# Performance work log

Hardware: AMD Instinct MI355X
Metric: run time of the kernel (lower is better)

The kernel has to match this reference:

```python
import jax, jax.numpy as jnp
import numpy as np

N = 50000      # nodes
E = 320000     # edges, sorted by relation, equal sections of E//R
R = 16         # num_rels
B = 8          # num_bases
IN = 256
OUT = 256


def setup_inputs() -> dict:
    key = jax.random.key(0)
    ks = jax.random.split(key, 7)
    feat = jax.random.normal(ks[0], (N, IN), dtype=jnp.float32)
    weight = jax.random.normal(ks[1], (B, IN, OUT), dtype=jnp.float32) * 0.05
    w_comp = jax.random.normal(ks[2], (R, B), dtype=jnp.float32) * 0.3
    loop_weight = jax.random.normal(ks[3], (IN, OUT), dtype=jnp.float32) * 0.05
    h_bias = jnp.zeros((OUT,), dtype=jnp.float32)
    norm = jax.random.uniform(ks[4], (E, 1), dtype=jnp.float32)
    src_idx = jax.random.randint(ks[5], (E,), 0, N)
    dst_idx = jax.random.randint(ks[6], (E,), 0, N)
    # edges sorted by relation type, equal-size sections (static for jit)
    etypes = jnp.repeat(jnp.arange(R), E // R)
    return dict(feat=feat, weight=weight, w_comp=w_comp, loop_weight=loop_weight,
                h_bias=h_bias, norm=norm, src_idx=src_idx, dst_idx=dst_idx,
                etypes=etypes)


def reference(feat, weight, w_comp, loop_weight, h_bias, norm, src_idx, dst_idx, etypes):
    # basis composition: per-relation weight [R, IN, OUT]
    w_rel = (w_comp @ weight.reshape(B, IN * OUT)).reshape(R, IN, OUT)
    # gather src features per edge; edges are grouped by relation (etypes sorted)
    h_src = feat[src_idx].reshape(R, E // R, IN)        # grouped GEMM operand
    msg = jnp.einsum('rei,rio->reo', h_src, w_rel).reshape(E, OUT)
    msg = msg * norm                                     # edge norm scaling
    # scatter-sum aggregation to dst nodes (fn.sum via update_all)
    node_repr = jax.ops.segment_sum(msg, dst_idx, num_segments=N)
    node_repr = node_repr + h_bias + feat @ loop_weight  # bias + self-loop
    return jax.nn.relu(node_repr)
```

## Files before the change

### kernel.cpp

```cpp
#include <hip/hip_runtime.h>

#define N_    50000
#define E_    320000
#define R_    16
#define B_    8
#define IN_   256
#define OUT_  256
#define EPR_  (E_ / R_)
#define MBLK_ 157
#define NBLK_ 391
#define SBLK_ 196

typedef float  f32x16 __attribute__((ext_vector_type(16)));
typedef __bf16 bf16x8 __attribute__((ext_vector_type(8)));

static __device__ __forceinline__ short f2bf(float f) {
  unsigned u = __float_as_uint(f);
  u = (u + 0x7FFFu + ((u >> 16) & 1u)) >> 16;
  return (short)u;
}
static __device__ __forceinline__ float bf2f(unsigned short s) {
  return __uint_as_float(((unsigned)s) << 16);
}

static __device__ __forceinline__ void gl_lds16(const short* g, short* l) {
  __builtin_amdgcn_global_load_lds(
      (const __attribute__((address_space(1))) void*)g,
      (__attribute__((address_space(3))) void*)l, 16, 0, 0);
}

__global__ void prep_kernel(const float* __restrict__ feat, const float* __restrict__ weight,
                            const float* __restrict__ w_comp, const float* __restrict__ loop_w,
                            short* __restrict__ w_relT, short* __restrict__ loopT,
                            short* __restrict__ feat_bf, int* __restrict__ counts) {
  int gid = blockIdx.x * blockDim.x + threadIdx.x;
  int gsz = gridDim.x * blockDim.x;
  for (int idx = gid; idx < R_ * OUT_ * IN_; idx += gsz) {
    int r = idx >> 16, i = (idx >> 8) & 255, o = idx & 255;
    float s = 0.f;
#pragma unroll
    for (int b = 0; b < B_; ++b)
      s += w_comp[r * B_ + b] * weight[(b * IN_ + i) * OUT_ + o];
    w_relT[(r * OUT_ + o) * IN_ + i] = f2bf(s);
  }
  for (int idx = gid; idx < OUT_ * IN_; idx += gsz) {
    int i = idx >> 8, o = idx & 255;
    loopT[o * IN_ + i] = f2bf(loop_w[i * OUT_ + o]);
  }
  for (int idx = gid; idx < (N_ * IN_) / 4; idx += gsz) {
    float4 v = ((const float4*)feat)[idx];
    short4 s4;
    s4.x = f2bf(v.x); s4.y = f2bf(v.y); s4.z = f2bf(v.z); s4.w = f2bf(v.w);
    ((short4*)feat_bf)[idx] = s4;
  }
  for (int idx = gid; idx < N_; idx += gsz) counts[idx] = 0;
}

__global__ void reorder_kernel(const short* __restrict__ w_relT, short* __restrict__ w_relS) {
  int idx = blockIdx.x * 256 + threadIdx.x;
  if (idx >= R_ * OUT_ * IN_) return;
  int r = idx >> 16;
  int rem = idx & 65535;
  int half = rem >> 15;
  int stage = (rem >> 13) & 3;
  int c = (rem >> 3) & 1023;
  int j = rem & 7;
  int scol = c >> 3;
  int q = (c & 7) ^ (scol & 7);
  int o = (half << 7) + scol;
  int i = (stage << 6) + (q << 3) + j;
  w_relS[idx] = w_relT[((r << 8) + o) * IN_ + i];
}

__global__ void hist_kernel(const int* __restrict__ dst_idx, int* __restrict__ counts) {
  int e = blockIdx.x * 256 + threadIdx.x;
  if (e < E_) atomicAdd(&counts[dst_idx[e]], 1);
}

__global__ void scan1_kernel(const int* __restrict__ counts, int* __restrict__ offsets,
                             int* __restrict__ bsum) {
  __shared__ int tmp[256];
  int tid = threadIdx.x;
  int gid = blockIdx.x * 256 + tid;
  int v = (gid < N_) ? counts[gid] : 0;
  tmp[tid] = v;
  __syncthreads();
  for (int d = 1; d < 256; d <<= 1) {
    int add = (tid >= d) ? tmp[tid - d] : 0;
    __syncthreads();
    tmp[tid] += add;
    __syncthreads();
  }
  if (gid < N_) offsets[gid] = tmp[tid] - v;
  if (tid == 255) bsum[blockIdx.x] = tmp[255];
}

__global__ void scan2_kernel(int* __restrict__ bsum) {
  __shared__ int tmp[256];
  int tid = threadIdx.x;
  int v = (tid < SBLK_) ? bsum[tid] : 0;
  tmp[tid] = v;
  __syncthreads();
  for (int d = 1; d < 256; d <<= 1) {
    int add = (tid >= d) ? tmp[tid - d] : 0;
    __syncthreads();
    tmp[tid] += add;
    __syncthreads();
  }
  if (tid < SBLK_) bsum[tid] = tmp[tid] - v;
}

__global__ void scan3_kernel(int* __restrict__ offsets, const int* __restrict__ bsum,
                             int* __restrict__ woff) {
  int gid = blockIdx.x * 256 + threadIdx.x;
  if (gid < N_) {
    int o = offsets[gid] + bsum[blockIdx.x];
    offsets[gid] = o;
    woff[gid] = o;
  }
}

__global__ void scatter_kernel(const int* __restrict__ dst_idx, int* __restrict__ woff,
                               int* __restrict__ pos) {
  int e = blockIdx.x * 256 + threadIdx.x;
  if (e < E_) {
    int p = atomicAdd(&woff[dst_idx[e]], 1);
    pos[e] = p;
  }
}

template <int MODE>
__launch_bounds__(256)
__global__ void edge_kernel(const short* __restrict__ feat_bf, const short* __restrict__ w_relS,
                            const float* __restrict__ norm, const int* __restrict__ src_idx,
                            const int* __restrict__ dst_idx, const int* __restrict__ pos,
                            short* __restrict__ msg, float* __restrict__ acc_out) {
  __shared__ short lds_w[4 * 8192];
  int bid  = blockIdx.x;
  int r    = bid / MBLK_;
  int mblk = bid - r * MBLK_;
  int e0   = r * EPR_ + mblk * 128;
  int rows = EPR_ - mblk * 128; if (rows > 128) rows = 128;

  int tid = threadIdx.x;
  int lane = tid & 63, wave = tid >> 6;
  int lm = lane & 31, hi = lane >> 5;
  int wr = wave << 5;

  int erow = wr + lm;
  int eg   = e0 + (erow < rows ? erow : 0);
  int src  = src_idx[eg];
  const bf16x8* __restrict__ arow = (const bf16x8*)(feat_bf + (size_t)src * IN_);

  bf16x8 a[16];
#pragma unroll
  for (int i = 0; i < 16; ++i) a[i] = arow[2 * i + hi];

  float nr[16]; int er_ok[16]; int prow[16]; int db[16];
#pragma unroll
  for (int t = 0; t < 16; ++t) {
    int row = (t & 3) + ((t >> 2) << 3) + (hi << 2);
    int er  = wr + row;
    int ee  = e0 + (er < rows ? er : 0);
    nr[t]    = norm[ee];
    er_ok[t] = (er < rows);
    prow[t]  = (MODE == 0) ? pos[ee] : 0;
    db[t]    = dst_idx[ee] * OUT_;
  }

  const short* wt = w_relS + (size_t)(r << 1) * 32768;

#pragma unroll
  for (int h = 0; h < 2; ++h) {
    if (h == 1) __syncthreads();
#pragma unroll
    for (int j = 0; j < 16; ++j) {
      int chunk = (wave << 4) + j;
      gl_lds16(wt + h * 32768 + chunk * 512 + lane * 8, &lds_w[chunk * 512]);
    }

    f32x16 acc[4];
#pragma unroll
    for (int g = 0; g < 4; ++g)
#pragma unroll
      for (int t = 0; t < 16; ++t) acc[g][t] = 0.f;

    __syncthreads();

#pragma unroll
    for (int stage = 0; stage < 4; ++stage) {
      const short* lb = &lds_w[stage * 8192];
#pragma unroll
      for (int s = 0; s < 4; ++s) {
        bf16x8 af = a[stage * 4 + s];
        int q = s * 2 + hi;
#pragma unroll
        for (int g = 0; g < 4; ++g) {
          int col = (g << 5) + lm;
          bf16x8 bfr = *(const bf16x8*)(&lb[col * 64 + ((q ^ (col & 7)) << 3)]);
          acc[g] = __builtin_amdgcn_mfma_f32_32x32x16_bf16(af, bfr, acc[g], 0, 0, 0);
        }
      }
    }

#pragma unroll
    for (int g = 0; g < 4; ++g) {
      int col = h * 128 + (g << 5) + lm;
#pragma unroll
      for (int t = 0; t < 16; ++t) {
        if (er_ok[t]) {
          float v = acc[g][t] * nr[t];
          if (MODE == 0)
            __builtin_nontemporal_store(f2bf(v), &msg[(size_t)prow[t] * OUT_ + col]);
          else
            unsafeAtomicAdd(&acc_out[(size_t)db[t] + col], v);
        }
      }
    }
  }
}

__launch_bounds__(256)
__global__ void agg_kernel(const short* __restrict__ msg, const int* __restrict__ offsets,
                           const int* __restrict__ counts, float* __restrict__ out) {
  int n = blockIdx.x * 4 + (threadIdx.x >> 6);
  if (n >= N_) return;
  int lane = threadIdx.x & 63;
  int off = offsets[n], cnt = counts[n];
  float4 a = make_float4(0.f, 0.f, 0.f, 0.f);
  const unsigned long long* __restrict__ m8 = (const unsigned long long*)msg;
  for (int j = 0; j < cnt; ++j) {
    unsigned long long v = __builtin_nontemporal_load(&m8[(size_t)(off + j) * 64 + lane]);
    a.x += bf2f((unsigned short)(v & 0xffffu));
    a.y += bf2f((unsigned short)((v >> 16) & 0xffffu));
    a.z += bf2f((unsigned short)((v >> 32) & 0xffffu));
    a.w += bf2f((unsigned short)(v >> 48));
  }
  ((float4*)out)[(size_t)n * 64 + lane] = a;
}

__global__ void zero_out_kernel(float* __restrict__ out) {
  int idx = blockIdx.x * 256 + threadIdx.x;
  if (idx < N_ * OUT_ / 4)
    ((float4*)out)[idx] = make_float4(0.f, 0.f, 0.f, 0.f);
}

__launch_bounds__(256)
__global__ void selfloop_kernel(const short* __restrict__ feat_bf, const short* __restrict__ loopT,
                                const float* __restrict__ h_bias, float* __restrict__ inout) {
  __shared__ short lds_b[128 * 64];
  int bid = blockIdx.x;
  int mblk = bid >> 1, nhalf = bid & 1;
  int n0 = mblk << 7;
  int rows = N_ - n0; if (rows > 128) rows = 128;

  int tid = threadIdx.x;
  int lane = tid & 63, wave = tid >> 6;
  int lm = lane & 31, hi = lane >> 5;
  int wr = wave << 5;

  int nrow = wr + lm;
  int ng = n0 + (nrow < rows ? nrow : 0);
  const bf16x8* __restrict__ arow = (const bf16x8*)(feat_bf + (size_t)ng * IN_);
  const short*  __restrict__ wb   = loopT + nhalf * 128 * IN_;

  f32x16 acc[4];
#pragma unroll
  for (int g = 0; g < 4; ++g)
#pragma unroll
    for (int t = 0; t < 16; ++t) acc[g][t] = 0.f;

  int scol = tid >> 1, sh = tid & 1;
  const bf16x8* __restrict__ gsrc0 = (const bf16x8*)(wb + scol * IN_ + sh * 32);

  for (int stage = 0; stage < 4; ++stage) {
#pragma unroll
    for (int c8 = 0; c8 < 4; ++c8) {
      int q = sh * 4 + c8;
      bf16x8 v = gsrc0[stage * 8 + c8];
      *(bf16x8*)(&lds_b[scol * 64 + ((q ^ (scol & 7)) << 3)]) = v;
    }
    bf16x8 af[4];
#pragma unroll
    for (int s = 0; s < 4; ++s) af[s] = arow[stage * 8 + s * 2 + hi];
    __syncthreads();
#pragma unroll
    for (int s = 0; s < 4; ++s) {
      int q = s * 2 + hi;
#pragma unroll
      for (int g = 0; g < 4; ++g) {
        int col = (g << 5) + lm;
        bf16x8 bfr = *(const bf16x8*)(&lds_b[col * 64 + ((q ^ (col & 7)) << 3)]);
        acc[g] = __builtin_amdgcn_mfma_f32_32x32x16_bf16(af[s], bfr, acc[g], 0, 0, 0);
      }
    }
    __syncthreads();
  }

#pragma unroll
  for (int g = 0; g < 4; ++g) {
    int col = nhalf * 128 + (g << 5) + lm;
    float hb = h_bias[col];
#pragma unroll
    for (int t = 0; t < 16; ++t) {
      int row = (t & 3) + ((t >> 2) << 3) + (hi << 2);
      int nn = wr + row;
      if (nn < rows) {
        size_t off = (size_t)(n0 + nn) * OUT_ + col;
        float x = inout[off] + acc[g][t] + hb;
        inout[off] = x > 0.f ? x : 0.f;
      }
    }
  }
}

extern "C" void kernel_launch(void* const* d_in, const int* in_sizes, int n_in,
                              void* d_out, int out_size, void* d_ws, size_t ws_size,
                              hipStream_t stream) {
  const float* feat    = (const float*)d_in[0];
  const float* weight  = (const float*)d_in[1];
  const float* w_comp  = (const float*)d_in[2];
  const float* loop_w  = (const float*)d_in[3];
  const float* h_bias  = (const float*)d_in[4];
  const float* norm    = (const float*)d_in[5];
  const int*   src_idx = (const int*)d_in[6];
  const int*   dst_idx = (const int*)d_in[7];
  float* out = (float*)d_out;

  short* w_relT  = (short*)d_ws;
  short* w_relS  = w_relT + R_ * OUT_ * IN_;
  short* loopT   = w_relS + R_ * OUT_ * IN_;
  short* feat_bf = loopT + OUT_ * IN_;
  int*   counts  = (int*)(feat_bf + (size_t)N_ * IN_);
  int*   offsets = counts + N_;
  int*   woff    = offsets + N_;
  int*   bsum    = woff + N_;
  int*   pos     = bsum + 256;
  short* msg     = (short*)(pos + E_);
  size_t need    = (size_t)((char*)(msg + (size_t)E_ * OUT_) - (char*)d_ws);

  prep_kernel<<<1024, 256, 0, stream>>>(feat, weight, w_comp, loop_w,
                                        w_relT, loopT, feat_bf, counts);
  reorder_kernel<<<(R_ * OUT_ * IN_) / 256, 256, 0, stream>>>(w_relT, w_relS);

  if (ws_size >= need) {
    hist_kernel<<<(E_ + 255) / 256, 256, 0, stream>>>(dst_idx, counts);
    scan1_kernel<<<SBLK_, 256, 0, stream>>>(counts, offsets, bsum);
    scan2_kernel<<<1, 256, 0, stream>>>(bsum);
    scan3_kernel<<<SBLK_, 256, 0, stream>>>(offsets, bsum, woff);
    scatter_kernel<<<(E_ + 255) / 256, 256, 0, stream>>>(dst_idx, woff, pos);
    edge_kernel<0><<<MBLK_ * R_, 256, 0, stream>>>(feat_bf, w_relS, norm, src_idx, dst_idx,
                                                   pos, msg, nullptr);
    agg_kernel<<<(N_ + 3) / 4, 256, 0, stream>>>(msg, offsets, counts, out);
  } else {
    zero_out_kernel<<<(N_ * OUT_ / 4 + 255) / 256, 256, 0, stream>>>(out);
    edge_kernel<1><<<MBLK_ * R_, 256, 0, stream>>>(feat_bf, w_relS, norm, src_idx, dst_idx,
                                                   nullptr, nullptr, out);
  }

  selfloop_kernel<<<NBLK_ * 2, 256, 0, stream>>>(feat_bf, loopT, h_bias, out);
}
```

Baseline: 235.7 us.

## Fold self-loop GEMM into edge kernel as extra relation and stage msg stores via LDS

The self-loop weight is treated as a 17th relation, so its GEMM runs as extra tiles of the edge kernel and writes into a reserved slot per destination node in the CSR message buffer. Bias and ReLU are then fused into the aggregation kernel, which removes the separate selfloop kernel and its read-modify-write of the fp32 output. Message stores now go through an LDS transpose so each thread writes 16-byte contiguous row chunks instead of scattered 2-byte stores. The cost is a larger message buffer (E+N rows) and the aggregation reading one extra row per node.

```diff
diff --git a/kernel.cpp b/kernel.cpp
--- a/kernel.cpp
+++ b/kernel.cpp
@@ -10,9 +10,11 @@
 #define MBLK_ 157
 #define NBLK_ 391
 #define SBLK_ 196
+#define TIL_  (R_ * MBLK_ + NBLK_)
 
 typedef float  f32x16 __attribute__((ext_vector_type(16)));
 typedef __bf16 bf16x8 __attribute__((ext_vector_type(8)));
+typedef unsigned uint4v __attribute__((ext_vector_type(4)));
 
 static __device__ __forceinline__ short f2bf(float f) {
   unsigned u = __float_as_uint(f);
@@ -31,8 +33,8 @@
 
 __global__ void prep_kernel(const float* __restrict__ feat, const float* __restrict__ weight,
                             const float* __restrict__ w_comp, const float* __restrict__ loop_w,
-                            short* __restrict__ w_relT, short* __restrict__ loopT,
-                            short* __restrict__ feat_bf, int* __restrict__ counts) {
+                            short* __restrict__ w_relT, short* __restrict__ feat_bf,
+                            int* __restrict__ counts) {
   int gid = blockIdx.x * blockDim.x + threadIdx.x;
   int gsz = gridDim.x * blockDim.x;
   for (int idx = gid; idx < R_ * OUT_ * IN_; idx += gsz) {
@@ -45,7 +47,7 @@
   }
   for (int idx = gid; idx < OUT_ * IN_; idx += gsz) {
     int i = idx >> 8, o = idx & 255;
-    loopT[o * IN_ + i] = f2bf(loop_w[i * OUT_ + o]);
+    w_relT[(R_ * OUT_ + o) * IN_ + i] = f2bf(loop_w[i * OUT_ + o]);
   }
   for (int idx = gid; idx < (N_ * IN_) / 4; idx += gsz) {
     float4 v = ((const float4*)feat)[idx];
@@ -58,7 +60,7 @@
 
 __global__ void reorder_kernel(const short* __restrict__ w_relT, short* __restrict__ w_relS) {
   int idx = blockIdx.x * 256 + threadIdx.x;
-  if (idx >= R_ * OUT_ * IN_) return;
+  if (idx >= (R_ + 1) * OUT_ * IN_) return;
   int r = idx >> 16;
   int rem = idx & 65535;
   int half = rem >> 15;
@@ -77,12 +79,12 @@
   if (e < E_) atomicAdd(&counts[dst_idx[e]], 1);
 }
 
-__global__ void scan1_kernel(const int* __restrict__ counts, int* __restrict__ offsets,
+__global__ void scan1_kernel(const int* __restrict__ counts, int* __restrict__ offc,
                              int* __restrict__ bsum) {
   __shared__ int tmp[256];
   int tid = threadIdx.x;
   int gid = blockIdx.x * 256 + tid;
-  int v = (gid < N_) ? counts[gid] : 0;
+  int v = (gid < N_) ? counts[gid] + 1 : 0;
   tmp[tid] = v;
   __syncthreads();
   for (int d = 1; d < 256; d <<= 1) {
@@ -91,7 +93,7 @@
     tmp[tid] += add;
     __syncthreads();
   }
-  if (gid < N_) offsets[gid] = tmp[tid] - v;
+  if (gid < N_) offc[gid] = tmp[tid] - v;
   if (tid == 255) bsum[blockIdx.x] = tmp[255];
 }
 
@@ -110,23 +112,20 @@
   if (tid < SBLK_) bsum[tid] = tmp[tid] - v;
 }
 
-__global__ void scan3_kernel(int* __restrict__ offsets, const int* __restrict__ bsum,
+__global__ void scan3_kernel(int* __restrict__ offc, const int* __restrict__ bsum,
                              int* __restrict__ woff) {
   int gid = blockIdx.x * 256 + threadIdx.x;
   if (gid < N_) {
-    int o = offsets[gid] + bsum[blockIdx.x];
-    offsets[gid] = o;
-    woff[gid] = o;
+    int o = offc[gid] + bsum[blockIdx.x];
+    offc[gid] = o;
+    woff[gid] = o + 1;
   }
 }
 
 __global__ void scatter_kernel(const int* __restrict__ dst_idx, int* __restrict__ woff,
                                int* __restrict__ pos) {
   int e = blockIdx.x * 256 + threadIdx.x;
-  if (e < E_) {
-    int p = atomicAdd(&woff[dst_idx[e]], 1);
-    pos[e] = p;
-  }
+  if (e < E_) pos[e] = atomicAdd(&woff[dst_idx[e]], 1);
 }
 
 template <int MODE>
@@ -134,13 +133,23 @@
 __global__ void edge_kernel(const short* __restrict__ feat_bf, const short* __restrict__ w_relS,
                             const float* __restrict__ norm, const int* __restrict__ src_idx,
                             const int* __restrict__ dst_idx, const int* __restrict__ pos,
-                            short* __restrict__ msg, float* __restrict__ acc_out) {
+                            const int* __restrict__ offc, short* __restrict__ msg,
+                            float* __restrict__ acc_out) {
   __shared__ short lds_w[4 * 8192];
-  int bid  = blockIdx.x;
-  int r    = bid / MBLK_;
-  int mblk = bid - r * MBLK_;
-  int e0   = r * EPR_ + mblk * 128;
-  int rows = EPR_ - mblk * 128; if (rows > 128) rows = 128;
+  int bid = blockIdx.x;
+  int r, mblk, e0, rows;
+  bool self;
+  if (bid < R_ * MBLK_) {
+    self = false;
+    r = bid / MBLK_; mblk = bid - r * MBLK_;
+    e0 = r * EPR_ + mblk * 128;
+    int lim = EPR_ - mblk * 128; rows = lim > 128 ? 128 : lim;
+  } else {
+    self = true;
+    r = R_; mblk = bid - R_ * MBLK_;
+    e0 = mblk * 128;
+    int lim = N_ - mblk * 128; rows = lim > 128 ? 128 : lim;
+  }
 
   int tid = threadIdx.x;
   int lane = tid & 63, wave = tid >> 6;
@@ -149,26 +158,23 @@
 
   int erow = wr + lm;
   int eg   = e0 + (erow < rows ? erow : 0);
-  int src  = src_idx[eg];
+  int src  = self ? eg : src_idx[eg];
   const bf16x8* __restrict__ arow = (const bf16x8*)(feat_bf + (size_t)src * IN_);
 
   bf16x8 a[16];
 #pragma unroll
   for (int i = 0; i < 16; ++i) a[i] = arow[2 * i + hi];
 
-  float nr[16]; int er_ok[16]; int prow[16]; int db[16];
+  float nr[16];
 #pragma unroll
   for (int t = 0; t < 16; ++t) {
     int row = (t & 3) + ((t >> 2) << 3) + (hi << 2);
     int er  = wr + row;
     int ee  = e0 + (er < rows ? er : 0);
-    nr[t]    = norm[ee];
-    er_ok[t] = (er < rows);
-    prow[t]  = (MODE == 0) ? pos[ee] : 0;
-    db[t]    = dst_idx[ee] * OUT_;
-  }
-
-  const short* wt = w_relS + (size_t)(r << 1) * 32768;
+    nr[t] = self ? 1.f : norm[ee];
+  }
+
+  const short* wt = w_relS + (size_t)r * 65536;
 
 #pragma unroll
   for (int h = 0; h < 2; ++h) {
@@ -203,17 +209,44 @@
       }
     }
 
-#pragma unroll
-    for (int g = 0; g < 4; ++g) {
-      int col = h * 128 + (g << 5) + lm;
-#pragma unroll
-      for (int t = 0; t < 16; ++t) {
-        if (er_ok[t]) {
-          float v = acc[g][t] * nr[t];
-          if (MODE == 0)
-            __builtin_nontemporal_store(f2bf(v), &msg[(size_t)prow[t] * OUT_ + col]);
-          else
-            unsafeAtomicAdd(&acc_out[(size_t)db[t] + col], v);
+    if (MODE == 0) {
+      __syncthreads();
+#pragma unroll
+      for (int g = 0; g < 4; ++g) {
+#pragma unroll
+        for (int t = 0; t < 16; ++t) {
+          int row = wr + (t & 3) + ((t >> 2) << 3) + (hi << 2);
+          int col = (g << 5) + lm;
+          int cs  = (col >> 3) ^ (row & 15);
+          lds_w[row * 128 + (cs << 3) + (col & 7)] = f2bf(acc[g][t] * nr[t]);
+        }
+      }
+      __syncthreads();
+      int row = tid >> 1, p = tid & 1;
+      if (row < rows) {
+        int ee = e0 + row;
+        int pr = self ? offc[ee] : pos[ee];
+        size_t mo = (size_t)pr * OUT_ + h * 128 + p * 64;
+#pragma unroll
+        for (int k = 0; k < 8; ++k) {
+          int c  = (p << 3) + k;
+          int cs = c ^ (row & 15);
+          uint4v v = *(const uint4v*)(&lds_w[row * 128 + (cs << 3)]);
+          __builtin_nontemporal_store(v, (uint4v*)(&msg[mo + (k << 3)]));
+        }
+      }
+    } else {
+#pragma unroll
+      for (int g = 0; g < 4; ++g) {
+#pragma unroll
+        for (int t = 0; t < 16; ++t) {
+          int row = (t & 3) + ((t >> 2) << 3) + (hi << 2);
+          int er  = wr + row;
+          if (er < rows) {
+            int ee = e0 + er;
+            int d  = (self ? ee : dst_idx[ee]) * OUT_ + h * 128 + (g << 5) + lm;
+            unsafeAtomicAdd(&acc_out[(size_t)d], acc[g][t] * nr[t]);
+          }
         }
       }
     }
@@ -221,12 +254,13 @@
 }
 
 __launch_bounds__(256)
-__global__ void agg_kernel(const short* __restrict__ msg, const int* __restrict__ offsets,
-                           const int* __restrict__ counts, float* __restrict__ out) {
+__global__ void agg_kernel(const short* __restrict__ msg, const int* __restrict__ offc,
+                           const int* __restrict__ counts, const float* __restrict__ h_bias,
+                           float* __restrict__ out) {
   int n = blockIdx.x * 4 + (threadIdx.x >> 6);
   if (n >= N_) return;
   int lane = threadIdx.x & 63;
-  int off = offsets[n], cnt = counts[n];
+  int off = offc[n], cnt = counts[n] + 1;
   float4 a = make_float4(0.f, 0.f, 0.f, 0.f);
   const unsigned long long* __restrict__ m8 = (const unsigned long long*)msg;
   for (int j = 0; j < cnt; ++j) {
@@ -236,6 +270,11 @@
     a.z += bf2f((unsigned short)((v >> 32) & 0xffffu));
     a.w += bf2f((unsigned short)(v >> 48));
   }
+  float4 b = ((const float4*)h_bias)[lane];
+  a.x = fmaxf(a.x + b.x, 0.f);
+  a.y = fmaxf(a.y + b.y, 0.f);
+  a.z = fmaxf(a.z + b.z, 0.f);
+  a.w = fmaxf(a.w + b.w, 0.f);
   ((float4*)out)[(size_t)n * 64 + lane] = a;
 }
 
@@ -244,73 +283,16 @@
   if (idx < N_ * OUT_ / 4)
     ((float4*)out)[idx] = make_float4(0.f, 0.f, 0.f, 0.f);
 }
-
-__launch_bounds__(256)
-__global__ void selfloop_kernel(const short* __restrict__ feat_bf, const short* __restrict__ loopT,
-                                const float* __restrict__ h_bias, float* __restrict__ inout) {
-  __shared__ short lds_b[128 * 64];
-  int bid = blockIdx.x;
-  int mblk = bid >> 1, nhalf = bid & 1;
-  int n0 = mblk << 7;
-  int rows = N_ - n0; if (rows > 128) rows = 128;
-
-  int tid = threadIdx.x;
-  int lane = tid & 63, wave = tid >> 6;
-  int lm = lane & 31, hi = lane >> 5;
-  int wr = wave << 5;
-
-  int nrow = wr + lm;
-  int ng = n0 + (nrow < rows ? nrow : 0);
-  const bf16x8* __restrict__ arow = (const bf16x8*)(feat_bf + (size_t)ng * IN_);
-  const short*  __restrict__ wb   = loopT + nhalf * 128 * IN_;
-
-  f32x16 acc[4];
-#pragma unroll
-  for (int g = 0; g < 4; ++g)
-#pragma unroll
-    for (int t = 0; t < 16; ++t) acc[g][t] = 0.f;
-
-  int scol = tid >> 1, sh = tid & 1;
-  const bf16x8* __restrict__ gsrc0 = (const bf16x8*)(wb + scol * IN_ + sh * 32);
-
-  for (int stage = 0; stage < 4; ++stage) {
-#pragma unroll
-    for (int c8 = 0; c8 < 4; ++c8) {
-      int q = sh * 4 + c8;
-      bf16x8 v = gsrc0[stage * 8 + c8];
-      *(bf16x8*)(&lds_b[scol * 64 + ((q ^ (scol & 7)) << 3)]) = v;
-    }
-    bf16x8 af[4];
-#pragma unroll
-    for (int s = 0; s < 4; ++s) af[s] = arow[stage * 8 + s * 2 + hi];
-    __syncthreads();
-#pragma unroll
-    for (int s = 0; s < 4; ++s) {
-      int q = s * 2 + hi;
-#pragma unroll
-      for (int g = 0; g < 4; ++g) {
-        int col = (g << 5) + lm;
-        bf16x8 bfr = *(const bf16x8*)(&lds_b[col * 64 + ((q ^ (col & 7)) << 3)]);
-        acc[g] = __builtin_amdgcn_mfma_f32_32x32x16_bf16(af[s], bfr, acc[g], 0, 0, 0);
-      }
-    }
-    __syncthreads();
-  }
-
-#pragma unroll
-  for (int g = 0; g < 4; ++g) {
-    int col = nhalf * 128 + (g << 5) + lm;
-    float hb = h_bias[col];
-#pragma unroll
-    for (int t = 0; t < 16; ++t) {
-      int row = (t & 3) + ((t >> 2) << 3) + (hi << 2);
-      int nn = wr + row;
-      if (nn < rows) {
-        size_t off = (size_t)(n0 + nn) * OUT_ + col;
-        float x = inout[off] + acc[g][t] + hb;
-        inout[off] = x > 0.f ? x : 0.f;
-      }
-    }
+__global__ void bias_relu_kernel(float* __restrict__ out, const float* __restrict__ h_bias) {
+  int idx = blockIdx.x * 256 + threadIdx.x;
+  if (idx < N_ * OUT_ / 4) {
+    float4 v = ((float4*)out)[idx];
+    float4 b = ((const float4*)h_bias)[idx & 63];
+    v.x = fmaxf(v.x + b.x, 0.f);
+    v.y = fmaxf(v.y + b.y, 0.f);
+    v.z = fmaxf(v.z + b.z, 0.f);
+    v.w = fmaxf(v.w + b.w, 0.f);
+    ((float4*)out)[idx] = v;
   }
 }
 
@@ -328,35 +310,33 @@
   float* out = (float*)d_out;
 
   short* w_relT  = (short*)d_ws;
-  short* w_relS  = w_relT + R_ * OUT_ * IN_;
-  short* loopT   = w_relS + R_ * OUT_ * IN_;
-  short* feat_bf = loopT + OUT_ * IN_;
+  short* w_relS  = w_relT + (R_ + 1) * OUT_ * IN_;
+  short* feat_bf = w_relS + (R_ + 1) * OUT_ * IN_;
   int*   counts  = (int*)(feat_bf + (size_t)N_ * IN_);
-  int*   offsets = counts + N_;
-  int*   woff    = offsets + N_;
+  int*   offc    = counts + N_;
+  int*   woff    = offc + N_;
   int*   bsum    = woff + N_;
   int*   pos     = bsum + 256;
   short* msg     = (short*)(pos + E_);
-  size_t need    = (size_t)((char*)(msg + (size_t)E_ * OUT_) - (char*)d_ws);
+  size_t need    = (size_t)((char*)(msg + (size_t)(E_ + N_) * OUT_) - (char*)d_ws);
 
   prep_kernel<<<1024, 256, 0, stream>>>(feat, weight, w_comp, loop_w,
-                                        w_relT, loopT, feat_bf, counts);
-  reorder_kernel<<<(R_ * OUT_ * IN_) / 256, 256, 0, stream>>>(w_relT, w_relS);
+                                        w_relT, feat_bf, counts);
+  reorder_kernel<<<((R_ + 1) * OUT_ * IN_) / 256, 256, 0, stream>>>(w_relT, w_relS);
+  hist_kernel<<<(E_ + 255) / 256, 256, 0, stream>>>(dst_idx, counts);
+  scan1_kernel<<<SBLK_, 256, 0, stream>>>(counts, offc, bsum);
+  scan2_kernel<<<1, 256, 0, stream>>>(bsum);
+  scan3_kernel<<<SBLK_, 256, 0, stream>>>(offc, bsum, woff);
+  scatter_kernel<<<(E_ + 255) / 256, 256, 0, stream>>>(dst_idx, woff, pos);
 
   if (ws_size >= need) {
-    hist_kernel<<<(E_ + 255) / 256, 256, 0, stream>>>(dst_idx, counts);
-    scan1_kernel<<<SBLK_, 256, 0, stream>>>(counts, offsets, bsum);
-    scan2_kernel<<<1, 256, 0, stream>>>(bsum);
-    scan3_kernel<<<SBLK_, 256, 0, stream>>>(offsets, bsum, woff);
-    scatter_kernel<<<(E_ + 255) / 256, 256, 0, stream>>>(dst_idx, woff, pos);
-    edge_kernel<0><<<MBLK_ * R_, 256, 0, stream>>>(feat_bf, w_relS, norm, src_idx, dst_idx,
-                                                   pos, msg, nullptr);
-    agg_kernel<<<(N_ + 3) / 4, 256, 0, stream>>>(msg, offsets, counts, out);
+    edge_kernel<0><<<TIL_, 256, 0, stream>>>(feat_bf, w_relS, norm, src_idx, dst_idx,
+                                             pos, offc, msg, nullptr);
+    agg_kernel<<<(N_ + 3) / 4, 256, 0, stream>>>(msg, offc, counts, h_bias, out);
   } else {
     zero_out_kernel<<<(N_ * OUT_ / 4 + 255) / 256, 256, 0, stream>>>(out);
-    edge_kernel<1><<<MBLK_ * R_, 256, 0, stream>>>(feat_bf, w_relS, norm, src_idx, dst_idx,
-                                                   nullptr, nullptr, out);
-  }
-
-  selfloop_kernel<<<NBLK_ * 2, 256, 0, stream>>>(feat_bf, loopT, h_bias, out);
-}
+    edge_kernel<1><<<TIL_, 256, 0, stream>>>(feat_bf, w_relS, norm, src_idx, dst_idx,
+                                             nullptr, offc, nullptr, out);
+    bias_relu_kernel<<<(N_ * OUT_ / 4 + 255) / 256, 256, 0, stream>>>(out, h_bias);
+  }
+}
```

Result: slower. 511.5 us (+117.0%).
